# Kernel tuning notes

Measured on AMD Instinct MI355X. Metric: run time of the kernel, lower is better.

The kernel has to match this reference:

```python
import jax, jax.numpy as jnp
import numpy as np

B, T, TREF, NBINS, H = 4096, 8192, 8192, 50, 32  # np.linspace(lo,hi,50) -> 49 bins
EPS = 1e-10


def setup_inputs() -> dict:
    key = jax.random.key(0)
    k0, k1, k2, k3, k4, k5 = jax.random.split(key, 6)
    return {
        "current_returns": jax.random.normal(k0, (B, T), jnp.float32) * 0.02,
        "reference_returns": jax.random.normal(k1, (TREF,), jnp.float32) * 0.02,
        "w1": jax.random.normal(k2, (H, 1), jnp.float32) * 0.5,   # Linear(1, H).weight
        "b1": jax.random.normal(k3, (H,), jnp.float32) * 0.1,
        "w2": jax.random.normal(k4, (H, H), jnp.float32) * 0.1,   # Linear(H, H).weight
        "b2": jax.random.normal(k5, (H,), jnp.float32) * 0.1,
    }


def _kl_from_hists(ref, curr, ref_min, ref_max):
    # Faithful to InformationTheory.kl_divergence with n_bins=50 (49 equal-width bins).
    nb = NBINS - 1
    lo = jnp.minimum(ref_min, curr.min())
    hi = jnp.maximum(ref_max, curr.max())
    width = (hi - lo) / nb

    def hist_density(x):
        # np.histogram(x, bins=linspace(lo,hi,50), density=True); all x in [lo,hi],
        # right edge goes to last bin (handled by clip).
        idx = jnp.clip(jnp.floor((x - lo) / width).astype(jnp.int32), 0, nb - 1)
        counts = jnp.zeros(nb, jnp.float32).at[idx].add(1.0)
        return counts / (x.shape[0] * width)

    p = hist_density(ref) + EPS
    q = hist_density(curr) + EPS
    p = p / p.sum()
    q = q / q.sum()
    return jnp.sum(p * jnp.log(p / q))


def reference(current_returns, reference_returns, w1, b1, w2, b2):
    ref = reference_returns
    ref_min, ref_max = ref.min(), ref.max()
    kl = jax.vmap(lambda c: _kl_from_hists(ref, c, ref_min, ref_max))(current_returns)  # [B]
    kl = jax.lax.stop_gradient(kl)  # original detaches before building kl_tensor
    x = kl[:, None]                                  # [B, 1]
    h = jax.nn.relu(x @ w1.T + b1)                   # [B, H]
    encoded = h @ w2.T + b2                          # [B, H]
    return kl, encoded
```

## Files before the change

kernel.cpp:

```cpp
#include <hip/hip_runtime.h>
#include <math.h>

constexpr int T_LEN  = 8192;
constexpr int B_ROWS = 4096;
constexpr int NB     = 49;
constexpr int NC     = 32;
constexpr int HDIM   = 32;
constexpr int FBINS  = 8192;
constexpr float EPSF = 1e-10f;

constexpr int WS_CDF_OFF    = 8;
constexpr int WS_BINNED_OFF = 8208;

__global__ __launch_bounds__(256)
void ref_cdf_kernel(const float* __restrict__ ref, float* __restrict__ wsf) {
    __shared__ float sv[FBINS];
    __shared__ int   hist[FBINS];
    __shared__ int   tsum[256];
    __shared__ float rmn4[4], rmx4[4];
    const int tid  = threadIdx.x;
    const int lane = tid & 63;
    const int wave = tid >> 6;

    const float4* r4 = (const float4*)ref;
    float4* sv4 = (float4*)sv;
    float mn = 3.0e38f, mx = -3.0e38f;
    #pragma unroll
    for (int i = 0; i < 8; ++i) {
        float4 v = r4[tid + i * 256];
        sv4[tid + i * 256] = v;
        mn = fminf(mn, fminf(fminf(v.x, v.y), fminf(v.z, v.w)));
        mx = fmaxf(mx, fmaxf(fmaxf(v.x, v.y), fmaxf(v.z, v.w)));
    }
    for (int i = tid; i < FBINS; i += 256) hist[i] = 0;
    #pragma unroll
    for (int off = 32; off > 0; off >>= 1) {
        mn = fminf(mn, __shfl_xor(mn, off));
        mx = fmaxf(mx, __shfl_xor(mx, off));
    }
    if (lane == 0) { rmn4[wave] = mn; rmx4[wave] = mx; }
    __syncthreads();
    const float rmin = fminf(fminf(rmn4[0], rmn4[1]), fminf(rmn4[2], rmn4[3]));
    const float rmax = fmaxf(fmaxf(rmx4[0], rmx4[1]), fmaxf(rmx4[2], rmx4[3]));
    const float finv = (float)FBINS / (rmax - rmin);

    for (int i = tid; i < FBINS; i += 256) {
        int fb = min(max((int)floorf((sv[i] - rmin) * finv), 0), FBINS - 1);
        atomicAdd(&hist[fb], 1);
    }
    __syncthreads();

    const int base = tid * 32;
    int s = 0;
    #pragma unroll
    for (int i = 0; i < 32; ++i) { int h = hist[base + i]; hist[base + i] = s; s += h; }
    tsum[tid] = s;
    __syncthreads();
    for (int off = 1; off < 256; off <<= 1) {
        int v = (tid >= off) ? tsum[tid - off] : 0;
        __syncthreads();
        tsum[tid] += v;
        __syncthreads();
    }
    const int toff = (tid == 0) ? 0 : tsum[tid - 1];
    #pragma unroll
    for (int i = 0; i < 32; ++i) hist[base + i] += toff;
    __syncthreads();

    int* cdf = (int*)(wsf + WS_CDF_OFF);
    for (int i = tid; i < FBINS; i += 256) cdf[i] = hist[i];
    if (tid == 0) { cdf[FBINS] = T_LEN; wsf[0] = rmin; wsf[1] = rmax; }
    __syncthreads();

    float* binned = wsf + WS_BINNED_OFF;
    for (int i = tid; i < FBINS; i += 256) {
        float x = sv[i];
        int fb = min(max((int)floorf((x - rmin) * finv), 0), FBINS - 1);
        int pos = atomicAdd(&hist[fb], 1);
        binned[pos] = x;
    }
}

__global__ __launch_bounds__(256)
void kl_fused_kernel(const float* __restrict__ cur,
                     const float* __restrict__ wsf,
                     const float* __restrict__ w1,
                     const float* __restrict__ b1,
                     const float* __restrict__ w2,
                     const float* __restrict__ b2,
                     float* __restrict__ kl_out,
                     float* __restrict__ enc_out) {
    __shared__ unsigned hq[NC * NB];
    __shared__ float rmn[4], rmx[4];

    const int b    = blockIdx.x;
    const int tid  = threadIdx.x;
    const int lane = tid & 63;
    const int wave = tid >> 6;

    for (int i = tid; i < NC * NB; i += 256) hq[i] = 0u;

    const float4* src = (const float4*)(cur + (size_t)b * T_LEN);
    float4 v[8];
    float mn = 3.0e38f, mx = -3.0e38f;
    #pragma unroll
    for (int i = 0; i < 8; ++i) {
        v[i] = src[tid + i * 256];
        mn = fminf(mn, fminf(fminf(v[i].x, v[i].y), fminf(v[i].z, v[i].w)));
        mx = fmaxf(mx, fmaxf(fmaxf(v[i].x, v[i].y), fmaxf(v[i].z, v[i].w)));
    }
    #pragma unroll
    for (int off = 32; off > 0; off >>= 1) {
        mn = fminf(mn, __shfl_xor(mn, off));
        mx = fmaxf(mx, __shfl_xor(mx, off));
    }
    if (lane == 0) { rmn[wave] = mn; rmx[wave] = mx; }
    __syncthreads();

    const float rmin = wsf[0];
    const float rmax = wsf[1];
    const float cmin = fminf(fminf(rmn[0], rmn[1]), fminf(rmn[2], rmn[3]));
    const float cmax = fmaxf(fmaxf(rmx[0], rmx[1]), fmaxf(rmx[2], rmx[3]));
    const float lo = fminf(rmin, cmin);
    const float hi = fmaxf(rmax, cmax);
    const float width = (hi - lo) / (float)NB;

    const float winv = 1.0f / width;
    const float nlw  = -lo * winv;
    unsigned* myq = hq + (tid & (NC - 1)) * NB;
    #pragma unroll
    for (int i = 0; i < 8; ++i) {
        int i0 = min(max((int)floorf(fmaf(v[i].x, winv, nlw)), 0), NB - 1);
        int i1 = min(max((int)floorf(fmaf(v[i].y, winv, nlw)), 0), NB - 1);
        int i2 = min(max((int)floorf(fmaf(v[i].z, winv, nlw)), 0), NB - 1);
        int i3 = min(max((int)floorf(fmaf(v[i].w, winv, nlw)), 0), NB - 1);
        atomicAdd(&myq[i0], 1u);
        atomicAdd(&myq[i1], 1u);
        atomicAdd(&myq[i2], 1u);
        atomicAdd(&myq[i3], 1u);
    }
    __syncthreads();

    if (tid < 64) {
        const bool act = tid < NB;
        int C = T_LEN;
        if (tid < NB - 1) {
            const float kp1  = (float)(tid + 1);
            const float finv = (float)FBINS / (rmax - rmin);
            const int* cdf = (const int*)(wsf + WS_CDF_OFF);
            const float* binned = wsf + WS_BINNED_OFF;
            const float t = fmaf(width, kp1, lo);
            int fb = (int)floorf((t - rmin) * finv);
            int a  = min(max(fb - 2, 0), FBINS);
            int bb = min(max(fb + 3, 0), FBINS);
            int ia = cdf[a], ib = cdf[bb];
            C = ia;
            for (int i = ia; i < ib; i += 4) {
                float x0 = binned[i];
                float x1 = (i + 1 < ib) ? binned[i + 1] : 3.0e38f;
                float x2 = (i + 2 < ib) ? binned[i + 2] : 3.0e38f;
                float x3 = (i + 3 < ib) ? binned[i + 3] : 3.0e38f;
                C += ((x0 - lo) / width < kp1) ? 1 : 0;
                C += ((x1 - lo) / width < kp1) ? 1 : 0;
                C += ((x2 - lo) / width < kp1) ? 1 : 0;
                C += ((x3 - lo) / width < kp1) ? 1 : 0;
            }
        }
        int Cprev = __shfl_up(C, 1);
        if (tid == 0) Cprev = 0;

        float p = 0.0f, q = 0.0f;
        if (act) {
            unsigned sq = 0u;
            #pragma unroll
            for (int c = 0; c < NC; ++c) sq += hq[c * NB + tid];
            const float inv = 1.0f / ((float)T_LEN * width);
            p = (float)(C - Cprev) * inv + EPSF;
            q = (float)sq * inv + EPSF;
        }
        float P = p, Q = q;
        #pragma unroll
        for (int off = 32; off > 0; off >>= 1) {
            P += __shfl_xor(P, off);
            Q += __shfl_xor(Q, off);
        }
        float term = 0.0f;
        if (act) {
            const float pn = p / P;
            const float qn = q / Q;
            term = pn * logf(pn / qn);
        }
        #pragma unroll
        for (int off = 32; off > 0; off >>= 1) term += __shfl_xor(term, off);
        if (tid == 0) kl_out[b] = term;

        if (tid < HDIM) {
            const float k = term;
            float acc = b2[tid];
            #pragma unroll
            for (int t = 0; t < HDIM; ++t) {
                float h = fmaxf(fmaf(k, w1[t], b1[t]), 0.0f);
                acc = fmaf(h, w2[tid * HDIM + t], acc);
            }
            enc_out[(size_t)b * HDIM + tid] = acc;
        }
    }
}

extern "C" void kernel_launch(void* const* d_in, const int* in_sizes, int n_in,
                              void* d_out, int out_size, void* d_ws, size_t ws_size,
                              hipStream_t stream) {
    const float* cur = (const float*)d_in[0];
    const float* ref = (const float*)d_in[1];
    const float* w1  = (const float*)d_in[2];
    const float* b1  = (const float*)d_in[3];
    const float* w2  = (const float*)d_in[4];
    const float* b2  = (const float*)d_in[5];
    float* out = (float*)d_out;
    float* wsf = (float*)d_ws;

    ref_cdf_kernel<<<1, 256, 0, stream>>>(ref, wsf);
    kl_fused_kernel<<<B_ROWS, 256, 0, stream>>>(
        cur, wsf, w1, b1, w2, b2, out, out + B_ROWS);
}
```

Before: 43.15 us.

## Process four rows per block with register double-buffered prefetch and wave-parallel KL tail

The main kernel now handles four rows per block. It prefetches the next row into a second register buffer while histogramming the current one, and the per-row KL/CDF search and MLP tail run in parallel, one row per wave. The reference CDF kernel swaps its multi-barrier block scan for a wave-shuffle scan, pads the LDS histogram against bank conflicts, and drops floorf where values are non-negative. This aims to hide load latency and cut the serial single-wave tail, at the cost of more registers, a quarter as many blocks, and extra barriers per row.

```diff
diff --git a/kernel.cpp b/kernel.cpp
--- a/kernel.cpp
+++ b/kernel.cpp
@@ -7,16 +7,25 @@
 constexpr int NC     = 32;
 constexpr int HDIM   = 32;
 constexpr int FBINS  = 8192;
+constexpr int ROWS   = 4;
 constexpr float EPSF = 1e-10f;
 
 constexpr int WS_CDF_OFF    = 8;
 constexpr int WS_BINNED_OFF = 8208;
+
+#define HP(i) ((i) + ((i) >> 5))
+
+__device__ __forceinline__ void sync_lds() {
+    asm volatile("s_waitcnt lgkmcnt(0)" ::: "memory");
+    __builtin_amdgcn_s_barrier();
+    __builtin_amdgcn_sched_barrier(0);
+}
 
 __global__ __launch_bounds__(256)
 void ref_cdf_kernel(const float* __restrict__ ref, float* __restrict__ wsf) {
     __shared__ float sv[FBINS];
-    __shared__ int   hist[FBINS];
-    __shared__ int   tsum[256];
+    __shared__ int   hist[HP(FBINS)];
+    __shared__ int   wsum[4];
     __shared__ float rmn4[4], rmx4[4];
     const int tid  = threadIdx.x;
     const int lane = tid & 63;
@@ -32,7 +41,7 @@
         mn = fminf(mn, fminf(fminf(v.x, v.y), fminf(v.z, v.w)));
         mx = fmaxf(mx, fmaxf(fmaxf(v.x, v.y), fmaxf(v.z, v.w)));
     }
-    for (int i = tid; i < FBINS; i += 256) hist[i] = 0;
+    for (int i = tid; i < HP(FBINS); i += 256) hist[i] = 0;
     #pragma unroll
     for (int off = 32; off > 0; off >>= 1) {
         mn = fminf(mn, __shfl_xor(mn, off));
@@ -45,165 +54,187 @@
     const float finv = (float)FBINS / (rmax - rmin);
 
     for (int i = tid; i < FBINS; i += 256) {
-        int fb = min(max((int)floorf((sv[i] - rmin) * finv), 0), FBINS - 1);
-        atomicAdd(&hist[fb], 1);
+        int fb = min(max((int)((sv[i] - rmin) * finv), 0), FBINS - 1);
+        atomicAdd(&hist[HP(fb)], 1);
     }
     __syncthreads();
 
     const int base = tid * 32;
     int s = 0;
     #pragma unroll
-    for (int i = 0; i < 32; ++i) { int h = hist[base + i]; hist[base + i] = s; s += h; }
-    tsum[tid] = s;
-    __syncthreads();
-    for (int off = 1; off < 256; off <<= 1) {
-        int v = (tid >= off) ? tsum[tid - off] : 0;
-        __syncthreads();
-        tsum[tid] += v;
-        __syncthreads();
-    }
-    const int toff = (tid == 0) ? 0 : tsum[tid - 1];
-    #pragma unroll
-    for (int i = 0; i < 32; ++i) hist[base + i] += toff;
+    for (int j = 0; j < 32; ++j) {
+        int h = hist[HP(base + j)]; hist[HP(base + j)] = s; s += h;
+    }
+    const int own = s;
+    int incl = s;
+    #pragma unroll
+    for (int off = 1; off < 64; off <<= 1) {
+        int t = __shfl_up(incl, off);
+        if (lane >= off) incl += t;
+    }
+    if (lane == 63) wsum[wave] = incl;
+    __syncthreads();
+    int woff = 0;
+    #pragma unroll
+    for (int w = 0; w < 4; ++w) if (w < wave) woff += wsum[w];
+    const int add = woff + incl - own;
+    #pragma unroll
+    for (int j = 0; j < 32; ++j) hist[HP(base + j)] += add;
     __syncthreads();
 
     int* cdf = (int*)(wsf + WS_CDF_OFF);
-    for (int i = tid; i < FBINS; i += 256) cdf[i] = hist[i];
+    for (int i = tid; i < FBINS; i += 256) cdf[i] = hist[HP(i)];
     if (tid == 0) { cdf[FBINS] = T_LEN; wsf[0] = rmin; wsf[1] = rmax; }
     __syncthreads();
 
     float* binned = wsf + WS_BINNED_OFF;
     for (int i = tid; i < FBINS; i += 256) {
         float x = sv[i];
-        int fb = min(max((int)floorf((x - rmin) * finv), 0), FBINS - 1);
-        int pos = atomicAdd(&hist[fb], 1);
+        int fb = min(max((int)((x - rmin) * finv), 0), FBINS - 1);
+        int pos = atomicAdd(&hist[HP(fb)], 1);
         binned[pos] = x;
     }
 }
 
 __global__ __launch_bounds__(256)
-void kl_fused_kernel(const float* __restrict__ cur,
-                     const float* __restrict__ wsf,
-                     const float* __restrict__ w1,
-                     const float* __restrict__ b1,
-                     const float* __restrict__ w2,
-                     const float* __restrict__ b2,
-                     float* __restrict__ kl_out,
-                     float* __restrict__ enc_out) {
+void kl_main_kernel(const float* __restrict__ cur,
+                    const float* __restrict__ wsf,
+                    const float* __restrict__ w1,
+                    const float* __restrict__ b1,
+                    const float* __restrict__ w2,
+                    const float* __restrict__ b2,
+                    float* __restrict__ kl_out,
+                    float* __restrict__ enc_out) {
     __shared__ unsigned hq[NC * NB];
-    __shared__ float rmn[4], rmx[4];
-
-    const int b    = blockIdx.x;
+    __shared__ float rmnS[4], rmxS[4];
+    __shared__ unsigned hrow[ROWS][NB];
+    __shared__ float metaLo[ROWS], metaW[ROWS];
+
     const int tid  = threadIdx.x;
     const int lane = tid & 63;
     const int wave = tid >> 6;
+    const int rbase = blockIdx.x * ROWS;
+    const float4* src = (const float4*)(cur + (size_t)rbase * T_LEN);
 
     for (int i = tid; i < NC * NB; i += 256) hq[i] = 0u;
-
-    const float4* src = (const float4*)(cur + (size_t)b * T_LEN);
-    float4 v[8];
-    float mn = 3.0e38f, mx = -3.0e38f;
-    #pragma unroll
-    for (int i = 0; i < 8; ++i) {
-        v[i] = src[tid + i * 256];
-        mn = fminf(mn, fminf(fminf(v[i].x, v[i].y), fminf(v[i].z, v[i].w)));
-        mx = fmaxf(mx, fmaxf(fmaxf(v[i].x, v[i].y), fmaxf(v[i].z, v[i].w)));
-    }
+    const float rmin = wsf[0], rmax = wsf[1];
+
+    float4 va[8], vb[8];
+    #pragma unroll
+    for (int i = 0; i < 8; ++i) va[i] = src[tid + i * 256];
+
+#define ROW_STEP(V, VN, R, PF)                                                 \
+    {                                                                          \
+        if (PF) {                                                              \
+            const float4* s2 = src + ((R) + 1) * (T_LEN / 4);                  \
+            _Pragma("unroll")                                                  \
+            for (int i = 0; i < 8; ++i) VN[i] = s2[tid + i * 256];             \
+        }                                                                      \
+        float mn = 3.0e38f, mx = -3.0e38f;                                     \
+        _Pragma("unroll")                                                      \
+        for (int i = 0; i < 8; ++i) {                                          \
+            mn = fminf(mn, fminf(fminf(V[i].x, V[i].y), fminf(V[i].z, V[i].w)));\
+            mx = fmaxf(mx, fmaxf(fmaxf(V[i].x, V[i].y), fmaxf(V[i].z, V[i].w)));\
+        }                                                                      \
+        _Pragma("unroll")                                                      \
+        for (int off = 32; off > 0; off >>= 1) {                               \
+            mn = fminf(mn, __shfl_xor(mn, off));                               \
+            mx = fmaxf(mx, __shfl_xor(mx, off));                               \
+        }                                                                      \
+        if (lane == 0) { rmnS[wave] = mn; rmxS[wave] = mx; }                   \
+        sync_lds();                                                            \
+        const float lo = fminf(rmin,                                           \
+            fminf(fminf(rmnS[0], rmnS[1]), fminf(rmnS[2], rmnS[3])));          \
+        const float hi = fmaxf(rmax,                                           \
+            fmaxf(fmaxf(rmxS[0], rmxS[1]), fmaxf(rmxS[2], rmxS[3])));          \
+        const float width = (hi - lo) / (float)NB;                             \
+        const float winv = 1.0f / width, nlw = -lo * winv;                     \
+        unsigned* myq = hq + (tid & (NC - 1)) * NB;                            \
+        _Pragma("unroll")                                                      \
+        for (int i = 0; i < 8; ++i) {                                          \
+            int i0 = min(max((int)fmaf(V[i].x, winv, nlw), 0), NB - 1);        \
+            int i1 = min(max((int)fmaf(V[i].y, winv, nlw), 0), NB - 1);        \
+            int i2 = min(max((int)fmaf(V[i].z, winv, nlw), 0), NB - 1);        \
+            int i3 = min(max((int)fmaf(V[i].w, winv, nlw), 0), NB - 1);        \
+            atomicAdd(&myq[i0], 1u); atomicAdd(&myq[i1], 1u);                  \
+            atomicAdd(&myq[i2], 1u); atomicAdd(&myq[i3], 1u);                  \
+        }                                                                      \
+        sync_lds();                                                            \
+        if (tid < 64 && lane < NB) {                                           \
+            unsigned sq = 0;                                                   \
+            _Pragma("unroll")                                                  \
+            for (int c = 0; c < NC; ++c) sq += hq[c * NB + lane];              \
+            hrow[R][lane] = sq;                                                \
+        }                                                                      \
+        if (tid == 0) { metaLo[R] = lo; metaW[R] = width; }                    \
+        sync_lds();                                                            \
+        for (int i = tid; i < NC * NB; i += 256) hq[i] = 0u;                   \
+    }
+
+    ROW_STEP(va, vb, 0, true)
+    ROW_STEP(vb, va, 1, true)
+    ROW_STEP(va, vb, 2, true)
+    ROW_STEP(vb, va, 3, false)
+#undef ROW_STEP
+
+    const int row = rbase + wave;
+    const float lo = metaLo[wave], width = metaW[wave];
+    const bool act = lane < NB;
+    const float inv = 1.0f / ((float)T_LEN * width);
+    float p = 0.0f, q = 0.0f;
+    if (act) q = (float)hrow[wave][lane] * inv + EPSF;
+
+    int C = T_LEN;
+    if (lane < NB - 1) {
+        const float kp1  = (float)(lane + 1);
+        const float finv = (float)FBINS / (rmax - rmin);
+        const int* cdf = (const int*)(wsf + WS_CDF_OFF);
+        const float* binned = wsf + WS_BINNED_OFF;
+        const float t = fmaf(width, kp1, lo);
+        int fb = (int)floorf((t - rmin) * finv);
+        int a  = min(max(fb - 2, 0), FBINS);
+        int bb = min(max(fb + 3, 0), FBINS);
+        int ia = cdf[a], ib = cdf[bb];
+        C = ia;
+        for (int i = ia; i < ib; i += 4) {
+            float x0 = binned[i];
+            float x1 = (i + 1 < ib) ? binned[i + 1] : 3.0e38f;
+            float x2 = (i + 2 < ib) ? binned[i + 2] : 3.0e38f;
+            float x3 = (i + 3 < ib) ? binned[i + 3] : 3.0e38f;
+            C += ((x0 - lo) / width < kp1) ? 1 : 0;
+            C += ((x1 - lo) / width < kp1) ? 1 : 0;
+            C += ((x2 - lo) / width < kp1) ? 1 : 0;
+            C += ((x3 - lo) / width < kp1) ? 1 : 0;
+        }
+    }
+    int Cprev = __shfl_up(C, 1);
+    if (lane == 0) Cprev = 0;
+    if (act) p = (float)(C - Cprev) * inv + EPSF;
+
+    float P = p, Q = q;
     #pragma unroll
     for (int off = 32; off > 0; off >>= 1) {
-        mn = fminf(mn, __shfl_xor(mn, off));
-        mx = fmaxf(mx, __shfl_xor(mx, off));
-    }
-    if (lane == 0) { rmn[wave] = mn; rmx[wave] = mx; }
-    __syncthreads();
-
-    const float rmin = wsf[0];
-    const float rmax = wsf[1];
-    const float cmin = fminf(fminf(rmn[0], rmn[1]), fminf(rmn[2], rmn[3]));
-    const float cmax = fmaxf(fmaxf(rmx[0], rmx[1]), fmaxf(rmx[2], rmx[3]));
-    const float lo = fminf(rmin, cmin);
-    const float hi = fmaxf(rmax, cmax);
-    const float width = (hi - lo) / (float)NB;
-
-    const float winv = 1.0f / width;
-    const float nlw  = -lo * winv;
-    unsigned* myq = hq + (tid & (NC - 1)) * NB;
-    #pragma unroll
-    for (int i = 0; i < 8; ++i) {
-        int i0 = min(max((int)floorf(fmaf(v[i].x, winv, nlw)), 0), NB - 1);
-        int i1 = min(max((int)floorf(fmaf(v[i].y, winv, nlw)), 0), NB - 1);
-        int i2 = min(max((int)floorf(fmaf(v[i].z, winv, nlw)), 0), NB - 1);
-        int i3 = min(max((int)floorf(fmaf(v[i].w, winv, nlw)), 0), NB - 1);
-        atomicAdd(&myq[i0], 1u);
-        atomicAdd(&myq[i1], 1u);
-        atomicAdd(&myq[i2], 1u);
-        atomicAdd(&myq[i3], 1u);
-    }
-    __syncthreads();
-
-    if (tid < 64) {
-        const bool act = tid < NB;
-        int C = T_LEN;
-        if (tid < NB - 1) {
-            const float kp1  = (float)(tid + 1);
-            const float finv = (float)FBINS / (rmax - rmin);
-            const int* cdf = (const int*)(wsf + WS_CDF_OFF);
-            const float* binned = wsf + WS_BINNED_OFF;
-            const float t = fmaf(width, kp1, lo);
-            int fb = (int)floorf((t - rmin) * finv);
-            int a  = min(max(fb - 2, 0), FBINS);
-            int bb = min(max(fb + 3, 0), FBINS);
-            int ia = cdf[a], ib = cdf[bb];
-            C = ia;
-            for (int i = ia; i < ib; i += 4) {
-                float x0 = binned[i];
-                float x1 = (i + 1 < ib) ? binned[i + 1] : 3.0e38f;
-                float x2 = (i + 2 < ib) ? binned[i + 2] : 3.0e38f;
-                float x3 = (i + 3 < ib) ? binned[i + 3] : 3.0e38f;
-                C += ((x0 - lo) / width < kp1) ? 1 : 0;
-                C += ((x1 - lo) / width < kp1) ? 1 : 0;
-                C += ((x2 - lo) / width < kp1) ? 1 : 0;
-                C += ((x3 - lo) / width < kp1) ? 1 : 0;
-            }
+        P += __shfl_xor(P, off);
+        Q += __shfl_xor(Q, off);
+    }
+    float term = 0.0f;
+    if (act) {
+        const float pn = p / P;
+        const float qn = q / Q;
+        term = pn * logf(pn / qn);
+    }
+    #pragma unroll
+    for (int off = 32; off > 0; off >>= 1) term += __shfl_xor(term, off);
+    if (lane == 0) kl_out[row] = term;
+
+    if (lane < HDIM) {
+        float acc = b2[lane];
+        #pragma unroll
+        for (int t2 = 0; t2 < HDIM; ++t2) {
+            float h = fmaxf(fmaf(term, w1[t2], b1[t2]), 0.0f);
+            acc = fmaf(h, w2[lane * HDIM + t2], acc);
         }
-        int Cprev = __shfl_up(C, 1);
-        if (tid == 0) Cprev = 0;
-
-        float p = 0.0f, q = 0.0f;
-        if (act) {
-            unsigned sq = 0u;
-            #pragma unroll
-            for (int c = 0; c < NC; ++c) sq += hq[c * NB + tid];
-            const float inv = 1.0f / ((float)T_LEN * width);
-            p = (float)(C - Cprev) * inv + EPSF;
-            q = (float)sq * inv + EPSF;
-        }
-        float P = p, Q = q;
-        #pragma unroll
-        for (int off = 32; off > 0; off >>= 1) {
-            P += __shfl_xor(P, off);
-            Q += __shfl_xor(Q, off);
-        }
-        float term = 0.0f;
-        if (act) {
-            const float pn = p / P;
-            const float qn = q / Q;
-            term = pn * logf(pn / qn);
-        }
-        #pragma unroll
-        for (int off = 32; off > 0; off >>= 1) term += __shfl_xor(term, off);
-        if (tid == 0) kl_out[b] = term;
-
-        if (tid < HDIM) {
-            const float k = term;
-            float acc = b2[tid];
-            #pragma unroll
-            for (int t = 0; t < HDIM; ++t) {
-                float h = fmaxf(fmaf(k, w1[t], b1[t]), 0.0f);
-                acc = fmaf(h, w2[tid * HDIM + t], acc);
-            }
-            enc_out[(size_t)b * HDIM + tid] = acc;
-        }
+        enc_out[(size_t)row * HDIM + lane] = acc;
     }
 }
 
@@ -220,6 +251,6 @@
     float* wsf = (float*)d_ws;
 
     ref_cdf_kernel<<<1, 256, 0, stream>>>(ref, wsf);
-    kl_fused_kernel<<<B_ROWS, 256, 0, stream>>>(
+    kl_main_kernel<<<B_ROWS / ROWS, 256, 0, stream>>>(
         cur, wsf, w1, b1, w2, b2, out, out + B_ROWS);
 }
```

New measurement: 44.50 us. +3.1%, slower.
